# Kernel optimization log

Measured on AMD Instinct MI355X. Metric: run time of the kernel, lower is better.

Reference implementation:

```python
import jax, jax.numpy as jnp
import numpy as np


def setup_inputs() -> dict:
    key = jax.random.key(0)
    k1, k2, k3, k4 = jax.random.split(key, 4)
    B, S, D, U = 4, 4096, 768, 64
    x = jax.random.normal(k1, (B, S, D), dtype=jnp.float32)
    mask = jax.random.randint(k2, (B, S), 0, 2) > 0  # bool [B,S]
    Wq = jax.random.normal(k3, (D, U), dtype=jnp.float32) * 0.02
    Wk = jax.random.normal(k4, (D, U), dtype=jnp.float32) * 0.02
    return {"x": x, "mask": mask, "Wq": Wq, "Wk": Wk}


def reference(x, mask, Wq, Wk):
    # Masked Linear (no bias): boolean_mask -> dense -> scatter_nd back with zeros
    # is equivalent to dense projection followed by zeroing masked positions.
    maskf = mask.astype(x.dtype)[..., None]            # [B,S,1]
    q = jnp.einsum('bsd,du->bsu', x, Wq) * maskf       # [B,S,U]
    k = jnp.einsum('bsd,du->bsu', x, Wk) * maskf       # [B,S,U]
    U = Wq.shape[-1]
    scale = 1.0 / jnp.sqrt(jnp.asarray(U, x.dtype))
    logits = jnp.einsum('bqu,bku->bqk', q, k) * scale  # [B,S,S]
    neg = jnp.asarray(-1e9, x.dtype)
    logits = jnp.where(mask[:, None, :], logits, neg)  # memory mask
    attn = jax.nn.softmax(logits, axis=-1)             # [B,S,S]
    out = jnp.einsum('bqk,bkd->bqd', attn, x)          # values are raw inputs
    out = out * maskf                                  # query mask zeros invalid rows
    return out
```

## Files before the change

### kernel.cpp

```cpp
#include <hip/hip_runtime.h>
#include <hip/hip_bf16.h>
#include <math.h>

#define B_ 4
#define S_ 4096
#define D_ 768
#define U_ 64
#define TK 32
#define NT (S_ / TK)
#define XT_TILE (TK * D_)
#define QK_TILE 2048
#define PSTR 776

typedef __attribute__((ext_vector_type(8))) short short8;
typedef __attribute__((ext_vector_type(16))) float f32x16;
typedef __attribute__((ext_vector_type(2))) unsigned int uint2v;

__device__ __forceinline__ unsigned short f2bf(float f) {
    unsigned int x = __float_as_uint(f);
    unsigned int r = (x + 0x7fffu + ((x >> 16) & 1u)) >> 16;
    return (unsigned short)r;
}

__global__ __launch_bounds__(256) void zero_k(float4* __restrict__ out, int n4) {
    int i = blockIdx.x * 256 + threadIdx.x;
    const int stride = gridDim.x * 256;
    const float4 z = make_float4(0.f, 0.f, 0.f, 0.f);
    for (; i < n4; i += stride) out[i] = z;
}

__global__ __launch_bounds__(256) void scan_k(const unsigned char* __restrict__ mraw,
                                              int* __restrict__ invK,
                                              int* __restrict__ nvbuf) {
    __shared__ int wsum[4];
    const int tid = threadIdx.x;
    const int b = blockIdx.x;
    int base = tid * 4;
    int bad = (mraw[base + 1] | mraw[base + 2] | mraw[base + 3]) != 0;
    int isbyte = __syncthreads_or(bad);
    int v[16]; int cnt = 0;
    const int s0 = tid * 16;
    #pragma unroll
    for (int e = 0; e < 16; ++e) {
        const int s = s0 + e;
        const int m = isbyte ? (int)mraw[b * S_ + s] : ((const int*)mraw)[b * S_ + s];
        v[e] = (m != 0); cnt += v[e];
    }
    int inc = cnt;
    #pragma unroll
    for (int off = 1; off < 64; off <<= 1) {
        const int y = __shfl_up(inc, off);
        if ((tid & 63) >= off) inc += y;
    }
    if ((tid & 63) == 63) wsum[tid >> 6] = inc;
    __syncthreads();
    int wbase = 0;
    #pragma unroll
    for (int ww = 0; ww < 4; ++ww) if (ww < (tid >> 6)) wbase += wsum[ww];
    int pos = wbase + inc - cnt;
    #pragma unroll
    for (int e = 0; e < 16; ++e)
        if (v[e]) { invK[b * S_ + pos] = s0 + e; ++pos; }
    if (tid == 255) nvbuf[b] = wbase + inc;
}

__global__ __launch_bounds__(256) void wfrag_k(const float* __restrict__ Wq,
                                               const float* __restrict__ Wk,
                                               unsigned short* __restrict__ wfg) {
    const int gid = blockIdx.x * 256 + threadIdx.x;
    const int fg = gid >> 6;
    const int l = gid & 63;
    const int m2 = fg / 96;
    const int rem = fg % 96;
    const int ut = rem / 48;
    const int kk = rem % 48;
    const float* __restrict__ W = m2 ? Wk : Wq;
    short8 v;
    #pragma unroll
    for (int e = 0; e < 8; ++e)
        v[e] = (short)f2bf(W[(kk * 16 + (l >> 5) * 8 + e) * U_ + ut * 32 + (l & 31)]);
    *(short8*)&wfg[(size_t)fg * 512 + l * 8] = v;
}

__global__ __launch_bounds__(256) void prep_k(const float* __restrict__ x,
                                              const int* __restrict__ invK,
                                              const int* __restrict__ nvbuf,
                                              const unsigned short* __restrict__ wfg,
                                              unsigned short* __restrict__ qg,
                                              unsigned short* __restrict__ kg,
                                              unsigned short* __restrict__ xTg) {
    const int blk = blockIdx.x;
    const int b = blk >> 7;
    const int ct = blk & 127;
    const int NV = nvbuf[b];
    if (ct * 32 >= NV) return;
    __shared__ unsigned short xs[32][PSTR];
    const int tid = threadIdx.x;
    {
        const int row = tid >> 3;
        const int c8 = tid & 7;
        const int cpos = min(ct * 32 + row, NV - 1);
        const int srow = invK[b * S_ + cpos];
        const float* xsrc = x + ((size_t)(b * S_ + srow)) * D_;
        #pragma unroll
        for (int it = 0; it < 24; ++it) {
            const int col = (c8 + it * 8) * 4;
            const float4 vv = *(const float4*)&xsrc[col];
            const unsigned int lo = __builtin_amdgcn_perm(
                __float_as_uint(vv.y) + 0x8000u, __float_as_uint(vv.x) + 0x8000u, 0x07060302u);
            const unsigned int hiw = __builtin_amdgcn_perm(
                __float_as_uint(vv.w) + 0x8000u, __float_as_uint(vv.z) + 0x8000u, 0x07060302u);
            *(uint2*)&xs[row][col] = make_uint2(lo, hiw);
        }
    }
    __syncthreads();
    {
        unsigned short* dst = xTg + (size_t)(b * NT + ct) * XT_TILE;
        #pragma unroll
        for (int it = 0; it < 12; ++it) {
            const int idx = it * 256 + tid;
            const int col = idx & 31;
            const int kh  = (idx >> 5) & 1;
            const int db  = (idx >> 6) % 24;
            const int kw  = idx / 1536;
            const int d   = db * 32 + col;
            const int sr  = kw * 16 + kh * 8;
            short8 v;
            #pragma unroll
            for (int e = 0; e < 8; ++e) v[e] = (short)xs[sr + e][d];
            *(short8*)&dst[idx * 8] = v;
        }
    }
    {
        const int w = tid >> 6;
        const int l = tid & 63;
        const unsigned short* wfb = wfg + (size_t)w * 48 * 512;
        f32x16 acc0 = {0.f}, acc1 = {0.f};
        #pragma unroll 4
        for (int kk = 0; kk < 48; kk += 2) {
            const short8 a0 = *(const short8*)&xs[l & 31][kk * 16 + (l >> 5) * 8];
            const short8 b0 = *(const short8*)&wfb[kk * 512 + l * 8];
            acc0 = __builtin_amdgcn_mfma_f32_32x32x16_bf16(a0, b0, acc0, 0, 0, 0);
            const short8 a1 = *(const short8*)&xs[l & 31][(kk + 1) * 16 + (l >> 5) * 8];
            const short8 b1 = *(const short8*)&wfb[(kk + 1) * 512 + l * 8];
            acc1 = __builtin_amdgcn_mfma_f32_32x32x16_bf16(a1, b1, acc1, 0, 0, 0);
        }
        const int ut = w & 1;
        unsigned short* dstqk = ((w >> 1) ? kg : qg) + (size_t)(b * NT + ct) * QK_TILE;
        const int mfrag = ut * 2 + ((l >> 4) & 1);
        const int b3 = (l >> 3) & 1;
        const int e  = l & 7;
        #pragma unroll
        for (int r = 0; r < 16; ++r) {
            const int row = (r & 3) + 8 * (r >> 2) + 4 * (l >> 5);
            dstqk[(mfrag * 64 + row + 32 * b3) * 8 + e] = f2bf(acc0[r] + acc1[r]);
        }
    }
}

__global__ __launch_bounds__(256, 3) void attn_k(const unsigned short* __restrict__ xTg,
                                                 const unsigned short* __restrict__ qg,
                                                 const unsigned short* __restrict__ kg,
                                                 const int* __restrict__ invK,
                                                 const int* __restrict__ nvbuf,
                                                 float* __restrict__ out) {
    __shared__ float sc_l[32];
    __shared__ float lsum[32];
    __shared__ int   is_l[32];
    __shared__ __align__(16) float am_l[2][64][20];

    const int tid = threadIdx.x;
    const int w = tid >> 6;
    const int l = tid & 63;
    const int hi = l >> 5;
    const int q5 = l & 31;
    const int ks = w >> 1;
    const int dg = w & 1;
    const int raw = blockIdx.x;
    const int bh = raw & 7;
    const int b = bh >> 1;
    const int par = bh & 1;
    const int idx = raw >> 3;
    const int dq = idx & 3;
    const int qt0 = ((idx >> 2) << 1) + par;
    const int db0 = dq * 6 + dg * 3;
    const int NV = nvbuf[b];
    const int ntc = (NV + 31) >> 5;
    const int htc = ntc >> 1;
    const int nfull_t = NV >> 5;

    const unsigned short* xT_b = xTg + (size_t)b * NT * XT_TILE;
    const unsigned short* kg_b = kg + (size_t)(b * NT) * QK_TILE;
    const float SCL2 = 0.125f * 1.4426950408889634f;

    const int nfull = ks ? (nfull_t - htc) : htc;
    const int tb = ks ? htc : 0;

    for (int qt = qt0; qt < NT; qt += 64) {
        if (qt * 32 >= NV) continue;
        const int q0 = qt * 32;

        short8 qf[4];
        {
            const unsigned short* qp = qg + (size_t)(b * NT + qt) * QK_TILE;
            #pragma unroll
            for (int m = 0; m < 4; ++m) qf[m] = *(const short8*)(qp + (m * 64 + l) * 8);
        }
        f32x16 acc[3];
        {
            f32x16 z = {0.f};
            #pragma unroll
            for (int j = 0; j < 3; ++j) acc[j] = z;
        }
        float l_run = 0.f;

        short8 kfA[4], kfB[4];
        {
            const unsigned short* kp = kg_b + (size_t)tb * QK_TILE;
            #pragma unroll
            for (int m = 0; m < 4; ++m) kfA[m] = *(const short8*)(kp + (m * 64 + l) * 8);
        }

        auto finish = [&](const f32x16& c, const short8 (&xv)[6], int kv) {
            float ps = 0.f;
            unsigned int W[8];
            #pragma unroll
            for (int j = 0; j < 8; ++j) {
                const int r0 = 2 * j, r1 = 2 * j + 1;
                float pa = exp2f(c[r0] * SCL2);
                float pb = exp2f(c[r1] * SCL2);
                if (kv < 32) {
                    const int k0 = (r0 & 3) + 8 * (r0 >> 2) + 4 * hi;
                    const int k1 = (r1 & 3) + 8 * (r1 >> 2) + 4 * hi;
                    pa = (k0 < kv) ? pa : 0.f;
                    pb = (k1 < kv) ? pb : 0.f;
                }
                ps += pa + pb;
                W[j] = __builtin_amdgcn_perm(__float_as_uint(pb), __float_as_uint(pa),
                                             0x07060302u);
            }
            ps += __shfl_xor(ps, 32);
            l_run += ps;
            const uint2v s02 = __builtin_amdgcn_permlane32_swap(W[0], W[2], false, false);
            const uint2v s13 = __builtin_amdgcn_permlane32_swap(W[1], W[3], false, false);
            const uint2v s46 = __builtin_amdgcn_permlane32_swap(W[4], W[6], false, false);
            const uint2v s57 = __builtin_amdgcn_permlane32_swap(W[5], W[7], false, false);
            union U4 { unsigned int u[4]; short8 v; };
            U4 a0, a1;
            a0.u[0] = s02.x; a0.u[1] = s13.x; a0.u[2] = s02.y; a0.u[3] = s13.y;
            a1.u[0] = s46.x; a1.u[1] = s57.x; a1.u[2] = s46.y; a1.u[3] = s57.y;
            #pragma unroll
            for (int j = 0; j < 3; ++j) {
                acc[j] = __builtin_amdgcn_mfma_f32_32x32x16_bf16(a0.v, xv[j], acc[j], 0, 0, 0);
                acc[j] = __builtin_amdgcn_mfma_f32_32x32x16_bf16(a1.v, xv[3 + j], acc[j], 0, 0, 0);
            }
        };

        auto step = [&](int tt, int tn, short8 (&kcur)[4], short8 (&knxt)[4]) {
            const unsigned short* xt = xT_b + (size_t)tt * XT_TILE;
            short8 xv[6];
            #pragma unroll
            for (int kw = 0; kw < 2; ++kw)
                #pragma unroll
                for (int j = 0; j < 3; ++j)
                    xv[kw * 3 + j] = *(const short8*)(xt + ((kw * 24 + db0 + j) * 64 + l) * 8);
            const unsigned short* kp = kg_b + (size_t)tn * QK_TILE;
            #pragma unroll
            for (int m = 0; m < 4; ++m) knxt[m] = *(const short8*)(kp + (m * 64 + l) * 8);
            f32x16 c = {0.f};
            #pragma unroll
            for (int m = 0; m < 4; ++m)
                c = __builtin_amdgcn_mfma_f32_32x32x16_bf16(kcur[m], qf[m], c, 0, 0, 0);
            finish(c, xv, 32);
        };

        int it = 0;
        for (; it + 1 < nfull; it += 2) {
            step(tb + it, tb + it + 1, kfA, kfB);
            step(tb + it + 1, (it + 2 < nfull) ? tb + it + 2 : tb, kfB, kfA);
        }
        if (it < nfull) step(tb + it, tb, kfA, kfB);

        if (ks && (NV & 31)) {
            const int tt = ntc - 1;
            short8 kp4[4];
            const unsigned short* kp = kg_b + (size_t)tt * QK_TILE;
            #pragma unroll
            for (int m = 0; m < 4; ++m) kp4[m] = *(const short8*)(kp + (m * 64 + l) * 8);
            const unsigned short* xt = xT_b + (size_t)tt * XT_TILE;
            short8 xv[6];
            #pragma unroll
            for (int kw = 0; kw < 2; ++kw)
                #pragma unroll
                for (int j = 0; j < 3; ++j)
                    xv[kw * 3 + j] = *(const short8*)(xt + ((kw * 24 + db0 + j) * 64 + l) * 8);
            f32x16 c = {0.f};
            #pragma unroll
            for (int m = 0; m < 4; ++m)
                c = __builtin_amdgcn_mfma_f32_32x32x16_bf16(kp4[m], qf[m], c, 0, 0, 0);
            finish(c, xv, NV & 31);
        }

        if (w == 2 && !hi) lsum[q5] = l_run;
        if (w == 0 && !hi) is_l[q5] = (q0 + q5 < NV) ? invK[b * S_ + q0 + q5] : -1;
        __syncthreads();
        if (w == 0 && !hi) {
            const float lt = l_run + lsum[q5];
            sc_l[q5] = (lt > 0.f) ? (1.f / lt) : 0.f;
        }
        __syncthreads();
        #pragma unroll
        for (int j = 0; j < 3; ++j) {
            if (ks) {
                #pragma unroll
                for (int g = 0; g < 4; ++g)
                    *(float4*)&am_l[dg][l][g * 4] =
                        make_float4(acc[j][g * 4 + 0], acc[j][g * 4 + 1],
                                    acc[j][g * 4 + 2], acc[j][g * 4 + 3]);
            }
            __syncthreads();
            if (!ks) {
                float4 iv[4];
                #pragma unroll
                for (int g = 0; g < 4; ++g) iv[g] = *(const float4*)&sc_l[g * 8 + hi * 4];
                const int dcol = (db0 + j) * 32 + q5;
                #pragma unroll
                for (int g = 0; g < 4; ++g) {
                    const float4 ab = *(const float4*)&am_l[dg][l][g * 4];
                    #pragma unroll
                    for (int e = 0; e < 4; ++e) {
                        const int r = g * 4 + e;
                        const int qr = (r & 3) + 8 * (r >> 2) + 4 * hi;
                        const int srow = is_l[qr];
                        if (srow >= 0)
                            out[(size_t)(b * S_ + srow) * D_ + dcol] =
                                (acc[j][r] + ((const float*)&ab)[e]) *
                                ((const float*)&iv[g])[e];
                    }
                }
            }
            __syncthreads();
        }
    }
}

extern "C" void kernel_launch(void* const* d_in, const int* in_sizes, int n_in,
                              void* d_out, int out_size, void* d_ws, size_t ws_size,
                              hipStream_t stream) {
    const float*         x    = (const float*)d_in[0];
    const unsigned char* mraw = (const unsigned char*)d_in[1];
    const float*         Wq   = (const float*)d_in[2];
    const float*         Wk   = (const float*)d_in[3];
    float*               outp = (float*)d_out;

    int* invK = (int*)d_ws;
    int* nvbuf = invK + (size_t)B_ * S_;
    unsigned short* qg  = (unsigned short*)(nvbuf + 16);
    unsigned short* kg  = qg + (size_t)B_ * S_ * U_;
    unsigned short* xTg = kg + (size_t)B_ * S_ * U_;
    unsigned short* wfg = xTg + (size_t)B_ * S_ * D_;

    zero_k<<<2048, 256, 0, stream>>>((float4*)outp, B_ * S_ * D_ / 4);
    scan_k<<<B_, 256, 0, stream>>>(mraw, invK, nvbuf);
    wfrag_k<<<48, 256, 0, stream>>>(Wq, Wk, wfg);
    prep_k<<<B_ * NT, 256, 0, stream>>>(x, invK, nvbuf, wfg, qg, kg, xTg);
    attn_k<<<1024, 256, 0, stream>>>(xTg, qg, kg, invK, nvbuf, outp);
}
```

Measured before the change: 126.8 us.

## Fuse setup kernels and split attention D across thirds with wider tiles

```diff
diff --git a/kernel.cpp b/kernel.cpp
--- a/kernel.cpp
+++ b/kernel.cpp
@@ -22,64 +22,65 @@
     return (unsigned short)r;
 }
 
-__global__ __launch_bounds__(256) void zero_k(float4* __restrict__ out, int n4) {
-    int i = blockIdx.x * 256 + threadIdx.x;
-    const int stride = gridDim.x * 256;
-    const float4 z = make_float4(0.f, 0.f, 0.f, 0.f);
-    for (; i < n4; i += stride) out[i] = z;
-}
-
-__global__ __launch_bounds__(256) void scan_k(const unsigned char* __restrict__ mraw,
-                                              int* __restrict__ invK,
-                                              int* __restrict__ nvbuf) {
-    __shared__ int wsum[4];
+__global__ __launch_bounds__(256) void fused0_k(const unsigned char* __restrict__ mraw,
+                                                const float* __restrict__ Wq,
+                                                const float* __restrict__ Wk,
+                                                int* __restrict__ invK,
+                                                int* __restrict__ nvbuf,
+                                                unsigned short* __restrict__ wfg,
+                                                float4* __restrict__ out, int n4) {
+    const int blk = blockIdx.x;
     const int tid = threadIdx.x;
-    const int b = blockIdx.x;
-    int base = tid * 4;
-    int bad = (mraw[base + 1] | mraw[base + 2] | mraw[base + 3]) != 0;
-    int isbyte = __syncthreads_or(bad);
-    int v[16]; int cnt = 0;
-    const int s0 = tid * 16;
-    #pragma unroll
-    for (int e = 0; e < 16; ++e) {
-        const int s = s0 + e;
-        const int m = isbyte ? (int)mraw[b * S_ + s] : ((const int*)mraw)[b * S_ + s];
-        v[e] = (m != 0); cnt += v[e];
-    }
-    int inc = cnt;
-    #pragma unroll
-    for (int off = 1; off < 64; off <<= 1) {
-        const int y = __shfl_up(inc, off);
-        if ((tid & 63) >= off) inc += y;
-    }
-    if ((tid & 63) == 63) wsum[tid >> 6] = inc;
-    __syncthreads();
-    int wbase = 0;
-    #pragma unroll
-    for (int ww = 0; ww < 4; ++ww) if (ww < (tid >> 6)) wbase += wsum[ww];
-    int pos = wbase + inc - cnt;
-    #pragma unroll
-    for (int e = 0; e < 16; ++e)
-        if (v[e]) { invK[b * S_ + pos] = s0 + e; ++pos; }
-    if (tid == 255) nvbuf[b] = wbase + inc;
-}
-
-__global__ __launch_bounds__(256) void wfrag_k(const float* __restrict__ Wq,
-                                               const float* __restrict__ Wk,
-                                               unsigned short* __restrict__ wfg) {
-    const int gid = blockIdx.x * 256 + threadIdx.x;
-    const int fg = gid >> 6;
-    const int l = gid & 63;
-    const int m2 = fg / 96;
-    const int rem = fg % 96;
-    const int ut = rem / 48;
-    const int kk = rem % 48;
-    const float* __restrict__ W = m2 ? Wk : Wq;
-    short8 v;
-    #pragma unroll
-    for (int e = 0; e < 8; ++e)
-        v[e] = (short)f2bf(W[(kk * 16 + (l >> 5) * 8 + e) * U_ + ut * 32 + (l & 31)]);
-    *(short8*)&wfg[(size_t)fg * 512 + l * 8] = v;
+    if (blk < 4) {
+        __shared__ int wsum[4];
+        const int b = blk;
+        int base = tid * 4;
+        int bad = (mraw[base + 1] | mraw[base + 2] | mraw[base + 3]) != 0;
+        int isbyte = __syncthreads_or(bad);
+        int v[16]; int cnt = 0;
+        const int s0 = tid * 16;
+        #pragma unroll
+        for (int e = 0; e < 16; ++e) {
+            const int s = s0 + e;
+            const int m = isbyte ? (int)mraw[b * S_ + s] : ((const int*)mraw)[b * S_ + s];
+            v[e] = (m != 0); cnt += v[e];
+        }
+        int inc = cnt;
+        #pragma unroll
+        for (int off = 1; off < 64; off <<= 1) {
+            const int y = __shfl_up(inc, off);
+            if ((tid & 63) >= off) inc += y;
+        }
+        if ((tid & 63) == 63) wsum[tid >> 6] = inc;
+        __syncthreads();
+        int wbase = 0;
+        #pragma unroll
+        for (int ww = 0; ww < 4; ++ww) if (ww < (tid >> 6)) wbase += wsum[ww];
+        int pos = wbase + inc - cnt;
+        #pragma unroll
+        for (int e = 0; e < 16; ++e)
+            if (v[e]) { invK[b * S_ + pos] = s0 + e; ++pos; }
+        if (tid == 255) nvbuf[b] = wbase + inc;
+    } else if (blk < 52) {
+        const int gid = (blk - 4) * 256 + tid;
+        const int fg = gid >> 6;
+        const int l = gid & 63;
+        const int m2 = fg / 96;
+        const int rem = fg % 96;
+        const int ut = rem / 48;
+        const int kk = rem % 48;
+        const float* __restrict__ W = m2 ? Wk : Wq;
+        short8 v;
+        #pragma unroll
+        for (int e = 0; e < 8; ++e)
+            v[e] = (short)f2bf(W[(kk * 16 + (l >> 5) * 8 + e) * U_ + ut * 32 + (l & 31)]);
+        *(short8*)&wfg[(size_t)fg * 512 + l * 8] = v;
+    } else {
+        int i = (blk - 52) * 256 + tid;
+        const int stride = (gridDim.x - 52) * 256;
+        const float4 z = make_float4(0.f, 0.f, 0.f, 0.f);
+        for (; i < n4; i += stride) out[i] = z;
+    }
 }
 
 __global__ __launch_bounds__(256) void prep_k(const float* __restrict__ x,
@@ -181,9 +182,10 @@
     const int b = bh >> 1;
     const int par = bh & 1;
     const int idx = raw >> 3;
-    const int dq = idx & 3;
-    const int qt0 = ((idx >> 2) << 1) + par;
-    const int db0 = dq * 6 + dg * 3;
+    const int dthird = idx % 3;
+    const int qtp = idx / 3;
+    const int qt0 = (qtp << 1) + par;
+    const int db0 = dthird * 8 + dg * 4;
     const int NV = nvbuf[b];
     const int ntc = (NV + 31) >> 5;
     const int htc = ntc >> 1;
@@ -206,11 +208,11 @@
             #pragma unroll
             for (int m = 0; m < 4; ++m) qf[m] = *(const short8*)(qp + (m * 64 + l) * 8);
         }
-        f32x16 acc[3];
+        f32x16 acc[4];
         {
             f32x16 z = {0.f};
             #pragma unroll
-            for (int j = 0; j < 3; ++j) acc[j] = z;
+            for (int j = 0; j < 4; ++j) acc[j] = z;
         }
         float l_run = 0.f;
 
@@ -221,7 +223,7 @@
             for (int m = 0; m < 4; ++m) kfA[m] = *(const short8*)(kp + (m * 64 + l) * 8);
         }
 
-        auto finish = [&](const f32x16& c, const short8 (&xv)[6], int kv) {
+        auto finish = [&](const f32x16& c, const short8 (&xv)[8], int kv) {
             float ps = 0.f;
             unsigned int W[8];
             #pragma unroll
@@ -250,20 +252,20 @@
             a0.u[0] = s02.x; a0.u[1] = s13.x; a0.u[2] = s02.y; a0.u[3] = s13.y;
             a1.u[0] = s46.x; a1.u[1] = s57.x; a1.u[2] = s46.y; a1.u[3] = s57.y;
             #pragma unroll
-            for (int j = 0; j < 3; ++j) {
+            for (int j = 0; j < 4; ++j) {
                 acc[j] = __builtin_amdgcn_mfma_f32_32x32x16_bf16(a0.v, xv[j], acc[j], 0, 0, 0);
-                acc[j] = __builtin_amdgcn_mfma_f32_32x32x16_bf16(a1.v, xv[3 + j], acc[j], 0, 0, 0);
+                acc[j] = __builtin_amdgcn_mfma_f32_32x32x16_bf16(a1.v, xv[4 + j], acc[j], 0, 0, 0);
             }
         };
 
         auto step = [&](int tt, int tn, short8 (&kcur)[4], short8 (&knxt)[4]) {
             const unsigned short* xt = xT_b + (size_t)tt * XT_TILE;
-            short8 xv[6];
+            short8 xv[8];
             #pragma unroll
             for (int kw = 0; kw < 2; ++kw)
                 #pragma unroll
-                for (int j = 0; j < 3; ++j)
-                    xv[kw * 3 + j] = *(const short8*)(xt + ((kw * 24 + db0 + j) * 64 + l) * 8);
+                for (int j = 0; j < 4; ++j)
+                    xv[kw * 4 + j] = *(const short8*)(xt + ((kw * 24 + db0 + j) * 64 + l) * 8);
             const unsigned short* kp = kg_b + (size_t)tn * QK_TILE;
             #pragma unroll
             for (int m = 0; m < 4; ++m) knxt[m] = *(const short8*)(kp + (m * 64 + l) * 8);
@@ -288,12 +290,12 @@
             #pragma unroll
             for (int m = 0; m < 4; ++m) kp4[m] = *(const short8*)(kp + (m * 64 + l) * 8);
             const unsigned short* xt = xT_b + (size_t)tt * XT_TILE;
-            short8 xv[6];
+            short8 xv[8];
             #pragma unroll
             for (int kw = 0; kw < 2; ++kw)
                 #pragma unroll
-                for (int j = 0; j < 3; ++j)
-                    xv[kw * 3 + j] = *(const short8*)(xt + ((kw * 24 + db0 + j) * 64 + l) * 8);
+                for (int j = 0; j < 4; ++j)
+                    xv[kw * 4 + j] = *(const short8*)(xt + ((kw * 24 + db0 + j) * 64 + l) * 8);
             f32x16 c = {0.f};
             #pragma unroll
             for (int m = 0; m < 4; ++m)
@@ -310,7 +312,7 @@
         }
         __syncthreads();
         #pragma unroll
-        for (int j = 0; j < 3; ++j) {
+        for (int j = 0; j < 4; ++j) {
             if (ks) {
                 #pragma unroll
                 for (int g = 0; g < 4; ++g)
@@ -360,9 +362,8 @@
     unsigned short* xTg = kg + (size_t)B_ * S_ * U_;
     unsigned short* wfg = xTg + (size_t)B_ * S_ * D_;
 
-    zero_k<<<2048, 256, 0, stream>>>((float4*)outp, B_ * S_ * D_ / 4);
-    scan_k<<<B_, 256, 0, stream>>>(mraw, invK, nvbuf);
-    wfrag_k<<<48, 256, 0, stream>>>(Wq, Wk, wfg);
+    fused0_k<<<2100, 256, 0, stream>>>(mraw, Wq, Wk, invK, nvbuf, wfg,
+                                       (float4*)outp, B_ * S_ * D_ / 4);
     prep_k<<<B_ * NT, 256, 0, stream>>>(x, invK, nvbuf, wfg, qg, kg, xTg);
-    attn_k<<<1024, 256, 0, stream>>>(xTg, qg, kg, invK, nvbuf, outp);
-}
+    attn_k<<<768, 256, 0, stream>>>(xTg, qg, kg, invK, nvbuf, outp);
+}
```

Result: slower. 187.1 us (+47.5%).
